# Kernel tuning notes

Hardware: AMD Instinct MI355X
Metric: run time of the kernel (lower is better)

The kernel has to match this reference:

```python
import jax, jax.numpy as jnp
import numpy as np

LEVEL = 2
IN_CH = 128
OUT_CH = 128
BASE_MODES = (16, 16)


def haar_dwt(x):
    # x: [B, C, H, W] with even H, W. Orthonormal 2D Haar (db1) analysis.
    x00 = x[:, :, 0::2, 0::2]
    x01 = x[:, :, 0::2, 1::2]
    x10 = x[:, :, 1::2, 0::2]
    x11 = x[:, :, 1::2, 1::2]
    ll = (x00 + x01 + x10 + x11) * 0.5
    lh = (x00 - x01 + x10 - x11) * 0.5  # high-freq along width
    hl = (x00 + x01 - x10 - x11) * 0.5  # high-freq along height
    hh = (x00 - x01 - x10 + x11) * 0.5
    return ll, lh, hl, hh


def haar_idwt(ll, lh, hl, hh):
    # Orthonormal 2D Haar synthesis (exact inverse of haar_dwt).
    x00 = (ll + lh + hl + hh) * 0.5
    x01 = (ll - lh + hl - hh) * 0.5
    x10 = (ll + lh - hl - hh) * 0.5
    x11 = (ll - lh - hl + hh) * 0.5
    b, c, h2, w2 = ll.shape
    row0 = jnp.stack([x00, x01], axis=-1).reshape(b, c, h2, 2 * w2)
    row1 = jnp.stack([x10, x11], axis=-1).reshape(b, c, h2, 2 * w2)
    return jnp.stack([row0, row1], axis=-2).reshape(b, c, 2 * h2, 2 * w2)


def setup_inputs() -> dict:
    key = jax.random.key(0)
    kx, k1, k2, k3, k4 = jax.random.split(key, 5)
    scale = 1.0 / (IN_CH * OUT_CH)
    wshape = (IN_CH, OUT_CH) + BASE_MODES
    x = jax.random.normal(kx, (32, IN_CH, 128, 128), dtype=jnp.float32)
    w1 = scale * jax.random.uniform(k1, wshape, dtype=jnp.float32)
    w2 = scale * jax.random.uniform(k2, wshape, dtype=jnp.float32)
    w3 = scale * jax.random.uniform(k3, wshape, dtype=jnp.float32)
    w4 = scale * jax.random.uniform(k4, wshape, dtype=jnp.float32)
    return {"x": x, "w1": w1, "w2": w2, "w3": w3, "w4": w4}


def reference(x, w1, w2, w3, w4):
    # Multi-level Haar DWT
    ll = x
    coeffs = []  # finest -> coarsest, matching pytorch_wavelets yh ordering
    for _ in range(LEVEL):
        ll, lh, hl, hh = haar_dwt(ll)
        coeffs.append((lh, hl, hh))

    th, tw = ll.shape[-2], ll.shape[-1]

    def interp(w):
        # bilinear, half-pixel centers == torch align_corners=False (upsampling)
        return jax.image.resize(w, w.shape[:2] + (th, tw), method="bilinear")

    def mul2d(a, w):
        return jnp.einsum("bixy,ioxy->boxy", a, interp(w))

    out_ll = mul2d(ll, w1)
    lh, hl, hh = coeffs[-1]  # only coarsest level is mixed; finer levels zeroed
    out = haar_idwt(out_ll, mul2d(lh, w2), mul2d(hl, w3), mul2d(hh, w4))
    for _ in range(LEVEL - 1):
        z = jnp.zeros_like(out)
        out = haar_idwt(out, z, z, z)
    return out
```

## Files before the change

kernel.cpp:

```cpp
#include <hip/hip_runtime.h>
#include <stdint.h>

__device__ __forceinline__ float bf2f(uint32_t v) { return __uint_as_float(v << 16); }
__device__ __forceinline__ uint32_t f2bf(float f) {
  uint32_t u = __float_as_uint(f);
  return (u + 0x7fffu + ((u >> 16) & 1u)) >> 16;
}

__device__ __forceinline__ void interp_coord(int p, int& i0, int& i1, float& f) {
  if (p == 0)       { i0 = 0;  i1 = 0;  f = 0.f; }
  else if (p == 31) { i0 = 15; i1 = 15; f = 0.f; }
  else if (p & 1)   { i0 = (p - 1) >> 1; i1 = i0 + 1; f = 0.25f; }
  else              { i0 = (p >> 1) - 1; i1 = i0 + 1; f = 0.75f; }
}

typedef short bf16x8 __attribute__((ext_vector_type(8)));
typedef float f32x4 __attribute__((ext_vector_type(4)));

__global__ __launch_bounds__(256) void dwt_kernel(const float* __restrict__ x,
                                                  uint16_t* __restrict__ bands) {
  __shared__ uint16_t tile[4 * 32 * 34];
  const int bid = blockIdx.x;
  const int cg4 = bid & 3;
  const int h   = (bid >> 2) & 31;
  const int b   = bid >> 7;
  const int t   = threadIdx.x;
  const int w   = t & 31;
  const int cl  = t >> 5;
#pragma unroll
  for (int cc = 0; cc < 4; ++cc) {
    const int c = cl + (cc << 3);
    const float* xc = x + (((size_t)(b << 7) + (cg4 << 5) + c) << 14) + (h << 9) + (w << 2);
    float4 r0 = *(const float4*)(xc);
    float4 r1 = *(const float4*)(xc + 128);
    float4 r2 = *(const float4*)(xc + 256);
    float4 r3 = *(const float4*)(xc + 384);
    float S00 = r0.x + r0.y + r1.x + r1.y;
    float S01 = r0.z + r0.w + r1.z + r1.w;
    float S10 = r2.x + r2.y + r3.x + r3.y;
    float S11 = r2.z + r2.w + r3.z + r3.w;
    tile[(0 * 32 + w) * 34 + c] = (uint16_t)f2bf(0.25f * (S00 + S01 + S10 + S11));
    tile[(1 * 32 + w) * 34 + c] = (uint16_t)f2bf(0.25f * (S00 - S01 + S10 - S11));
    tile[(2 * 32 + w) * 34 + c] = (uint16_t)f2bf(0.25f * (S00 + S01 - S10 - S11));
    tile[(3 * 32 + w) * 34 + c] = (uint16_t)f2bf(0.25f * (S00 - S01 - S10 + S11));
  }
  __syncthreads();
  const uint32_t* tl = (const uint32_t*)tile;
  uint32_t* bo = (uint32_t*)bands;
#pragma unroll
  for (int j = 0; j < 8; ++j) {
    const int idx = t + (j << 8);
    const int k   = idx >> 9;
    const int rem = idx & 511;
    const int w2  = rem >> 4;
    const int qq  = rem & 15;
    const uint32_t v = tl[(k * 32 + w2) * 17 + qq];
    bo[(((size_t)(k << 10) + (h << 5) + w2) << 11) + (b << 6) + (cg4 << 4) + qq] = v;
  }
}

__global__ __launch_bounds__(256) void wrepack_kernel(const float* __restrict__ w1,
                                                      const float* __restrict__ w2,
                                                      const float* __restrict__ w3,
                                                      const float* __restrict__ w4,
                                                      uint16_t* __restrict__ wr) {
  __shared__ uint16_t L[64 * 262];
  const int bid = blockIdx.x;
  const int k = bid >> 7;
  const int o = bid & 127;
  const float* src = (k == 0) ? w1 : (k == 1) ? w2 : (k == 2) ? w3 : w4;
  const int t = threadIdx.x;
  uint32_t* Lu = (uint32_t*)L;
  for (int ih = 0; ih < 2; ++ih) {
    if (ih) __syncthreads();
#pragma unroll
    for (int j = 0; j < 16; ++j) {
      const int ridx = t + (j << 8);
      const int il = ridx >> 6;
      const int x4 = ridx & 63;
      float4 v = *(const float4*)(src + (((size_t)((ih * 64 + il) * 128 + o)) << 8) + (x4 << 2));
      Lu[il * 131 + (x4 << 1)]     = f2bf(v.x) | (f2bf(v.y) << 16);
      Lu[il * 131 + (x4 << 1) + 1] = f2bf(v.z) | (f2bf(v.w) << 16);
    }
    __syncthreads();
#pragma unroll
    for (int j = 0; j < 32; ++j) {
      const int oidx = t + (j << 8);
      const int yx = oidx >> 5;
      const int q  = oidx & 31;
      const uint32_t lo = L[(q << 1) * 262 + yx];
      const uint32_t hi = L[((q << 1) + 1) * 262 + yx];
      uint32_t* dst = (uint32_t*)wr + (((size_t)(k << 8) + yx) << 13) + (o << 6) + (ih << 5) + q;
      *dst = lo | (hi << 16);
    }
  }
}

__global__ __launch_bounds__(256) void gemm_kernel(const uint16_t* __restrict__ bands,
                                                   const uint16_t* __restrict__ wr,
                                                   uint16_t* __restrict__ ws2) {
  __shared__ uint16_t Wt[128 * 136];
  const int bid = blockIdx.x;
  const int k = bid & 3;
  const int p = bid >> 2;
  const int t = threadIdx.x;
  const int py = p >> 5, px = p & 31;
  int y0, y1, x0, x1; float fy, fx;
  interp_coord(py, y0, y1, fy);
  interp_coord(px, x0, x1, fx);
  const float c00 = (1.f - fy) * (1.f - fx), c01 = (1.f - fy) * fx;
  const float c10 = fy * (1.f - fx),         c11 = fy * fx;
  const uint16_t* wk = wr + ((size_t)k << 22);
  const uint4* rA = (const uint4*)(wk + (((size_t)(y0 << 4) + x0) << 14));
  const uint4* rB = (const uint4*)(wk + (((size_t)(y0 << 4) + x1) << 14));
  const uint4* rC = (const uint4*)(wk + (((size_t)(y1 << 4) + x0) << 14));
  const uint4* rD = (const uint4*)(wk + (((size_t)(y1 << 4) + x1) << 14));
  uint32_t* Wtu = (uint32_t*)Wt;
#pragma unroll
  for (int j = 0; j < 8; ++j) {
    const int fi = t + (j << 8);
    const int o  = fi >> 4;
    const int i8 = fi & 15;
    const uint4 a = rA[fi], b = rB[fi], c = rC[fi], d = rD[fi];
    uint32_t ou[4];
#pragma unroll
    for (int cc = 0; cc < 4; ++cc) {
      const uint32_t ua = (&a.x)[cc], ub = (&b.x)[cc], uc = (&c.x)[cc], ud = (&d.x)[cc];
      float lo = c00 * __uint_as_float(ua << 16) + c01 * __uint_as_float(ub << 16)
               + c10 * __uint_as_float(uc << 16) + c11 * __uint_as_float(ud << 16);
      float hi = c00 * __uint_as_float(ua & 0xffff0000u) + c01 * __uint_as_float(ub & 0xffff0000u)
               + c10 * __uint_as_float(uc & 0xffff0000u) + c11 * __uint_as_float(ud & 0xffff0000u);
      ou[cc] = f2bf(lo) | (f2bf(hi) << 16);
    }
    *(uint4*)(Wtu + o * 68 + (i8 << 2)) = make_uint4(ou[0], ou[1], ou[2], ou[3]);
  }
  __syncthreads();
  const int wv = t >> 6;
  const int l  = t & 63;
  const int lr = l & 15;
  const int lk = (l >> 4) << 3;
  const uint16_t* gA = bands + (((size_t)(k << 10) + p) << 12);
  bf16x8 af[2][4], bg[2][4];
#pragma unroll
  for (int s = 0; s < 4; ++s) {
#pragma unroll
    for (int m = 0; m < 2; ++m)
      af[m][s] = *(const bf16x8*)(gA + (((m << 4) + lr) << 7) + (s << 5) + lk);
#pragma unroll
    for (int n = 0; n < 2; ++n)
      bg[n][s] = *(const bf16x8*)(&Wt[((wv << 5) + (n << 4) + lr) * 136 + (s << 5) + lk]);
  }
  f32x4 acc[2][2] = {};
#pragma unroll
  for (int s = 0; s < 4; ++s)
#pragma unroll
    for (int m = 0; m < 2; ++m)
#pragma unroll
      for (int n = 0; n < 2; ++n)
        acc[m][n] = __builtin_amdgcn_mfma_f32_16x16x32_bf16(af[m][s], bg[n][s], acc[m][n], 0, 0, 0);
  __syncthreads();
  uint16_t* Ds = Wt;
#pragma unroll
  for (int m = 0; m < 2; ++m)
#pragma unroll
    for (int n = 0; n < 2; ++n)
#pragma unroll
      for (int r = 0; r < 4; ++r) {
        const int b_ = (m << 4) + ((l >> 4) << 2) + r;
        const int o_ = (wv << 5) + (n << 4) + lr;
        Ds[b_ * 136 + o_] = (uint16_t)f2bf(acc[m][n][r]);
      }
  __syncthreads();
  uint32_t* outp = (uint32_t*)(ws2 + (((size_t)(k << 10) + p) << 12));
  const uint32_t* Dsu = (const uint32_t*)Ds;
#pragma unroll
  for (int j = 0; j < 8; ++j) {
    const int idx = t + (j << 8);
    const int b_ = idx >> 6, c_ = idx & 63;
    outp[idx] = Dsu[b_ * 68 + c_];
  }
}

__global__ __launch_bounds__(256) void idwt_kernel(const uint16_t* __restrict__ ws2,
                                                   float* __restrict__ out) {
  __shared__ uint16_t Ls[4 * 32 * 130];
  const int bid = blockIdx.x;
  const int b = bid >> 5;
  const int h = bid & 31;
  const int t = threadIdx.x;
  const uint32_t* su = (const uint32_t*)ws2;
  uint32_t* Lu = (uint32_t*)Ls;
#pragma unroll 4
  for (int j = 0; j < 32; ++j) {
    const int idx = t + (j << 8);
    const int kw = idx >> 6;
    const int uo = idx & 63;
    const int k = kw >> 5, w = kw & 31;
    const uint32_t v = su[(((size_t)(k << 10) + (h << 5) + w) << 11) + (b << 6) + uo];
    Lu[kw * 65 + uo] = v;
  }
  __syncthreads();
  const int x4 = t & 31;
  const int og = t >> 5;
  for (int pp = 0; pp < 16; ++pp) {
    const int o = (pp << 3) + og;
    const float A = bf2f(Ls[(0 * 32 + x4) * 130 + o]);
    const float B = bf2f(Ls[(1 * 32 + x4) * 130 + o]);
    const float C = bf2f(Ls[(2 * 32 + x4) * 130 + o]);
    const float D = bf2f(Ls[(3 * 32 + x4) * 130 + o]);
    const float E = A + B, F = A - B, G = C + D, Hh = C - D;
    const float vL0 = 0.25f * (E + G),  vR0 = 0.25f * (F + Hh);
    const float vL1 = 0.25f * (E - G),  vR1 = 0.25f * (F - Hh);
    float* ob = out + (((size_t)(b << 7) + o) << 14) + (h << 9) + (x4 << 2);
    float4 top = make_float4(vL0, vL0, vR0, vR0);
    float4 bot = make_float4(vL1, vL1, vR1, vR1);
    *(float4*)(ob)       = top;
    *(float4*)(ob + 128) = top;
    *(float4*)(ob + 256) = bot;
    *(float4*)(ob + 384) = bot;
  }
}

extern "C" void kernel_launch(void* const* d_in, const int* in_sizes, int n_in,
                              void* d_out, int out_size, void* d_ws, size_t ws_size,
                              hipStream_t stream) {
  const float* x  = (const float*)d_in[0];
  const float* w1 = (const float*)d_in[1];
  const float* w2 = (const float*)d_in[2];
  const float* w3 = (const float*)d_in[3];
  const float* w4 = (const float*)d_in[4];

  uint16_t* bands = (uint16_t*)d_ws;
  uint16_t* ws2   = bands + (size_t)16777216;
  uint16_t* wr = (uint16_t*)d_out;

  wrepack_kernel<<<512, 256, 0, stream>>>(w1, w2, w3, w4, wr);
  dwt_kernel<<<4096, 256, 0, stream>>>(x, bands);
  gemm_kernel<<<4096, 256, 0, stream>>>(bands, wr, ws2);
  idwt_kernel<<<1024, 256, 0, stream>>>(ws2, (float*)d_out);
}
```

Before: 557.5 us.

## Merge weight repack into DWT kernel and share weight corners across four GEMM positions

```diff
diff --git a/kernel.cpp b/kernel.cpp
--- a/kernel.cpp
+++ b/kernel.cpp
@@ -17,81 +17,80 @@
 typedef short bf16x8 __attribute__((ext_vector_type(8)));
 typedef float f32x4 __attribute__((ext_vector_type(4)));
 
-__global__ __launch_bounds__(256) void dwt_kernel(const float* __restrict__ x,
-                                                  uint16_t* __restrict__ bands) {
-  __shared__ uint16_t tile[4 * 32 * 34];
-  const int bid = blockIdx.x;
-  const int cg4 = bid & 3;
-  const int h   = (bid >> 2) & 31;
-  const int b   = bid >> 7;
-  const int t   = threadIdx.x;
-  const int w   = t & 31;
-  const int cl  = t >> 5;
-#pragma unroll
-  for (int cc = 0; cc < 4; ++cc) {
-    const int c = cl + (cc << 3);
-    const float* xc = x + (((size_t)(b << 7) + (cg4 << 5) + c) << 14) + (h << 9) + (w << 2);
-    float4 r0 = *(const float4*)(xc);
-    float4 r1 = *(const float4*)(xc + 128);
-    float4 r2 = *(const float4*)(xc + 256);
-    float4 r3 = *(const float4*)(xc + 384);
-    float S00 = r0.x + r0.y + r1.x + r1.y;
-    float S01 = r0.z + r0.w + r1.z + r1.w;
-    float S10 = r2.x + r2.y + r3.x + r3.y;
-    float S11 = r2.z + r2.w + r3.z + r3.w;
-    tile[(0 * 32 + w) * 34 + c] = (uint16_t)f2bf(0.25f * (S00 + S01 + S10 + S11));
-    tile[(1 * 32 + w) * 34 + c] = (uint16_t)f2bf(0.25f * (S00 - S01 + S10 - S11));
-    tile[(2 * 32 + w) * 34 + c] = (uint16_t)f2bf(0.25f * (S00 + S01 - S10 - S11));
-    tile[(3 * 32 + w) * 34 + c] = (uint16_t)f2bf(0.25f * (S00 - S01 - S10 + S11));
-  }
-  __syncthreads();
-  const uint32_t* tl = (const uint32_t*)tile;
-  uint32_t* bo = (uint32_t*)bands;
-#pragma unroll
-  for (int j = 0; j < 8; ++j) {
-    const int idx = t + (j << 8);
-    const int k   = idx >> 9;
-    const int rem = idx & 511;
-    const int w2  = rem >> 4;
-    const int qq  = rem & 15;
-    const uint32_t v = tl[(k * 32 + w2) * 17 + qq];
-    bo[(((size_t)(k << 10) + (h << 5) + w2) << 11) + (b << 6) + (cg4 << 4) + qq] = v;
-  }
-}
-
-__global__ __launch_bounds__(256) void wrepack_kernel(const float* __restrict__ w1,
-                                                      const float* __restrict__ w2,
-                                                      const float* __restrict__ w3,
-                                                      const float* __restrict__ w4,
-                                                      uint16_t* __restrict__ wr) {
-  __shared__ uint16_t L[64 * 262];
-  const int bid = blockIdx.x;
-  const int k = bid >> 7;
-  const int o = bid & 127;
-  const float* src = (k == 0) ? w1 : (k == 1) ? w2 : (k == 2) ? w3 : w4;
+__global__ __launch_bounds__(256) void front_kernel(const float* __restrict__ x,
+                                                    const float* __restrict__ w1,
+                                                    const float* __restrict__ w2,
+                                                    const float* __restrict__ w3,
+                                                    const float* __restrict__ w4,
+                                                    uint16_t* __restrict__ bands,
+                                                    uint16_t* __restrict__ wr) {
+  __shared__ uint16_t sh[64 * 262];
   const int t = threadIdx.x;
-  uint32_t* Lu = (uint32_t*)L;
-  for (int ih = 0; ih < 2; ++ih) {
-    if (ih) __syncthreads();
-#pragma unroll
-    for (int j = 0; j < 16; ++j) {
-      const int ridx = t + (j << 8);
-      const int il = ridx >> 6;
-      const int x4 = ridx & 63;
-      float4 v = *(const float4*)(src + (((size_t)((ih * 64 + il) * 128 + o)) << 8) + (x4 << 2));
-      Lu[il * 131 + (x4 << 1)]     = f2bf(v.x) | (f2bf(v.y) << 16);
-      Lu[il * 131 + (x4 << 1) + 1] = f2bf(v.z) | (f2bf(v.w) << 16);
-    }
-    __syncthreads();
-#pragma unroll
-    for (int j = 0; j < 32; ++j) {
-      const int oidx = t + (j << 8);
-      const int yx = oidx >> 5;
-      const int q  = oidx & 31;
-      const uint32_t lo = L[(q << 1) * 262 + yx];
-      const uint32_t hi = L[((q << 1) + 1) * 262 + yx];
-      uint32_t* dst = (uint32_t*)wr + (((size_t)(k << 8) + yx) << 13) + (o << 6) + (ih << 5) + q;
-      *dst = lo | (hi << 16);
+  if (blockIdx.x < 512) {
+    const int bid = blockIdx.x;
+    const int k = bid >> 7;
+    const int o = bid & 127;
+    const float* src = (k == 0) ? w1 : (k == 1) ? w2 : (k == 2) ? w3 : w4;
+    uint32_t* Lu = (uint32_t*)sh;
+    for (int ih = 0; ih < 2; ++ih) {
+      if (ih) __syncthreads();
+#pragma unroll
+      for (int j = 0; j < 16; ++j) {
+        const int ridx = t + (j << 8);
+        const int il = ridx >> 6;
+        const int x4 = ridx & 63;
+        float4 v = *(const float4*)(src + (((size_t)((ih * 64 + il) * 128 + o)) << 8) + (x4 << 2));
+        Lu[il * 131 + (x4 << 1)]     = f2bf(v.x) | (f2bf(v.y) << 16);
+        Lu[il * 131 + (x4 << 1) + 1] = f2bf(v.z) | (f2bf(v.w) << 16);
+      }
+      __syncthreads();
+#pragma unroll
+      for (int j = 0; j < 32; ++j) {
+        const int oidx = t + (j << 8);
+        const int yx = oidx >> 5;
+        const int q  = oidx & 31;
+        const uint32_t lo = sh[(q << 1) * 262 + yx];
+        const uint32_t hi = sh[((q << 1) + 1) * 262 + yx];
+        uint32_t* dst = (uint32_t*)wr + (((size_t)(k << 8) + yx) << 13) + (o << 6) + (ih << 5) + q;
+        *dst = lo | (hi << 16);
+      }
+    }
+  } else {
+    const int bid = blockIdx.x - 512;
+    const int cg4 = bid & 3;
+    const int h   = (bid >> 2) & 31;
+    const int b   = bid >> 7;
+    const int w   = t & 31;
+    const int cl  = t >> 5;
+#pragma unroll
+    for (int cc = 0; cc < 4; ++cc) {
+      const int c = cl + (cc << 3);
+      const float* xc = x + (((size_t)(b << 7) + (cg4 << 5) + c) << 14) + (h << 9) + (w << 2);
+      float4 r0 = *(const float4*)(xc);
+      float4 r1 = *(const float4*)(xc + 128);
+      float4 r2 = *(const float4*)(xc + 256);
+      float4 r3 = *(const float4*)(xc + 384);
+      float S00 = r0.x + r0.y + r1.x + r1.y;
+      float S01 = r0.z + r0.w + r1.z + r1.w;
+      float S10 = r2.x + r2.y + r3.x + r3.y;
+      float S11 = r2.z + r2.w + r3.z + r3.w;
+      sh[(0 * 32 + w) * 34 + c] = (uint16_t)f2bf(0.25f * (S00 + S01 + S10 + S11));
+      sh[(1 * 32 + w) * 34 + c] = (uint16_t)f2bf(0.25f * (S00 - S01 + S10 - S11));
+      sh[(2 * 32 + w) * 34 + c] = (uint16_t)f2bf(0.25f * (S00 + S01 - S10 - S11));
+      sh[(3 * 32 + w) * 34 + c] = (uint16_t)f2bf(0.25f * (S00 - S01 - S10 + S11));
+    }
+    __syncthreads();
+    const uint32_t* tl = (const uint32_t*)sh;
+    uint32_t* bo = (uint32_t*)bands;
+#pragma unroll
+    for (int j = 0; j < 8; ++j) {
+      const int idx = t + (j << 8);
+      const int k   = idx >> 9;
+      const int rem = idx & 511;
+      const int w2  = rem >> 4;
+      const int qq  = rem & 15;
+      const uint32_t v = tl[(k * 32 + w2) * 17 + qq];
+      bo[(((size_t)(k << 10) + (h << 5) + w2) << 11) + (b << 6) + (cg4 << 4) + qq] = v;
     }
   }
 }
@@ -101,83 +100,104 @@
                                                    uint16_t* __restrict__ ws2) {
   __shared__ uint16_t Wt[128 * 136];
   const int bid = blockIdx.x;
-  const int k = bid & 3;
-  const int p = bid >> 2;
-  const int t = threadIdx.x;
-  const int py = p >> 5, px = p & 31;
-  int y0, y1, x0, x1; float fy, fx;
-  interp_coord(py, y0, y1, fy);
-  interp_coord(px, x0, x1, fx);
-  const float c00 = (1.f - fy) * (1.f - fx), c01 = (1.f - fy) * fx;
-  const float c10 = fy * (1.f - fx),         c11 = fy * fx;
+  const int lid = ((bid & 7) << 7) + (bid >> 3);
+  const int xg = lid & 15;
+  const int yg = (lid >> 4) & 15;
+  const int k  = lid >> 8;
+  int pys[2], pxs[2], ya, yb, xa, xb;
+  if (yg < 15) { pys[0] = 2 * yg + 1; pys[1] = 2 * yg + 2; ya = yg; yb = yg + 1; }
+  else         { pys[0] = 0;          pys[1] = 31;         ya = 0;  yb = 15;     }
+  if (xg < 15) { pxs[0] = 2 * xg + 1; pxs[1] = 2 * xg + 2; xa = xg; xb = xg + 1; }
+  else         { pxs[0] = 0;          pxs[1] = 31;         xa = 0;  xb = 15;     }
+  float WY[2][2], WX[2][2];
+#pragma unroll
+  for (int i = 0; i < 2; ++i) {
+    int y0_, y1_; float fy;
+    interp_coord(pys[i], y0_, y1_, fy);
+    WY[i][0] = (y0_ == ya ? (1.f - fy) : 0.f) + (y1_ == ya ? fy : 0.f);
+    WY[i][1] = (y0_ == yb ? (1.f - fy) : 0.f) + (y1_ == yb ? fy : 0.f);
+    int x0_, x1_; float fx;
+    interp_coord(pxs[i], x0_, x1_, fx);
+    WX[i][0] = (x0_ == xa ? (1.f - fx) : 0.f) + (x1_ == xa ? fx : 0.f);
+    WX[i][1] = (x0_ == xb ? (1.f - fx) : 0.f) + (x1_ == xb ? fx : 0.f);
+  }
   const uint16_t* wk = wr + ((size_t)k << 22);
-  const uint4* rA = (const uint4*)(wk + (((size_t)(y0 << 4) + x0) << 14));
-  const uint4* rB = (const uint4*)(wk + (((size_t)(y0 << 4) + x1) << 14));
-  const uint4* rC = (const uint4*)(wk + (((size_t)(y1 << 4) + x0) << 14));
-  const uint4* rD = (const uint4*)(wk + (((size_t)(y1 << 4) + x1) << 14));
-  uint32_t* Wtu = (uint32_t*)Wt;
-#pragma unroll
-  for (int j = 0; j < 8; ++j) {
-    const int fi = t + (j << 8);
-    const int o  = fi >> 4;
-    const int i8 = fi & 15;
-    const uint4 a = rA[fi], b = rB[fi], c = rC[fi], d = rD[fi];
-    uint32_t ou[4];
-#pragma unroll
-    for (int cc = 0; cc < 4; ++cc) {
-      const uint32_t ua = (&a.x)[cc], ub = (&b.x)[cc], uc = (&c.x)[cc], ud = (&d.x)[cc];
-      float lo = c00 * __uint_as_float(ua << 16) + c01 * __uint_as_float(ub << 16)
-               + c10 * __uint_as_float(uc << 16) + c11 * __uint_as_float(ud << 16);
-      float hi = c00 * __uint_as_float(ua & 0xffff0000u) + c01 * __uint_as_float(ub & 0xffff0000u)
-               + c10 * __uint_as_float(uc & 0xffff0000u) + c11 * __uint_as_float(ud & 0xffff0000u);
-      ou[cc] = f2bf(lo) | (f2bf(hi) << 16);
-    }
-    *(uint4*)(Wtu + o * 68 + (i8 << 2)) = make_uint4(ou[0], ou[1], ou[2], ou[3]);
-  }
-  __syncthreads();
+  const uint4* rA = (const uint4*)wk + (size_t)((ya << 4) + xa) * 2048;
+  const uint4* rB = (const uint4*)wk + (size_t)((ya << 4) + xb) * 2048;
+  const uint4* rC = (const uint4*)wk + (size_t)((yb << 4) + xa) * 2048;
+  const uint4* rD = (const uint4*)wk + (size_t)((yb << 4) + xb) * 2048;
+  const int t  = threadIdx.x;
   const int wv = t >> 6;
   const int l  = t & 63;
   const int lr = l & 15;
   const int lk = (l >> 4) << 3;
-  const uint16_t* gA = bands + (((size_t)(k << 10) + p) << 12);
-  bf16x8 af[2][4], bg[2][4];
-#pragma unroll
-  for (int s = 0; s < 4; ++s) {
+  uint32_t* Wtu = (uint32_t*)Wt;
+#pragma unroll 1
+  for (int pp = 0; pp < 4; ++pp) {
+    const int iy = pp >> 1, ix = pp & 1;
+    const float c00 = WY[iy][0] * WX[ix][0], c01 = WY[iy][0] * WX[ix][1];
+    const float c10 = WY[iy][1] * WX[ix][0], c11 = WY[iy][1] * WX[ix][1];
+    const int p = (pys[iy] << 5) + pxs[ix];
+    if (pp) __syncthreads();
+#pragma unroll
+    for (int j = 0; j < 8; ++j) {
+      const int fi = t + (j << 8);
+      const int o  = fi >> 4;
+      const int i8 = fi & 15;
+      const uint4 a = rA[fi], b = rB[fi], c = rC[fi], d = rD[fi];
+      uint32_t ou[4];
+#pragma unroll
+      for (int cc = 0; cc < 4; ++cc) {
+        const uint32_t ua = (&a.x)[cc], ub = (&b.x)[cc], uc = (&c.x)[cc], ud = (&d.x)[cc];
+        float lo = c00 * __uint_as_float(ua << 16) + c01 * __uint_as_float(ub << 16)
+                 + c10 * __uint_as_float(uc << 16) + c11 * __uint_as_float(ud << 16);
+        float hi = c00 * __uint_as_float(ua & 0xffff0000u) + c01 * __uint_as_float(ub & 0xffff0000u)
+                 + c10 * __uint_as_float(uc & 0xffff0000u) + c11 * __uint_as_float(ud & 0xffff0000u);
+        ou[cc] = f2bf(lo) | (f2bf(hi) << 16);
+      }
+      *(uint4*)(Wtu + o * 68 + (i8 << 2)) = make_uint4(ou[0], ou[1], ou[2], ou[3]);
+    }
+    __syncthreads();
+    const uint16_t* gA = bands + (((size_t)(k << 10) + p) << 12);
+    bf16x8 af[2][4], bg[2][4];
+#pragma unroll
+    for (int s = 0; s < 4; ++s) {
+#pragma unroll
+      for (int m = 0; m < 2; ++m)
+        af[m][s] = *(const bf16x8*)(gA + (((m << 4) + lr) << 7) + (s << 5) + lk);
+#pragma unroll
+      for (int n = 0; n < 2; ++n)
+        bg[n][s] = *(const bf16x8*)(&Wt[((wv << 5) + (n << 4) + lr) * 136 + (s << 5) + lk]);
+    }
+    f32x4 acc[2][2] = {};
+#pragma unroll
+    for (int s = 0; s < 4; ++s)
+#pragma unroll
+      for (int m = 0; m < 2; ++m)
+#pragma unroll
+        for (int n = 0; n < 2; ++n)
+          acc[m][n] = __builtin_amdgcn_mfma_f32_16x16x32_bf16(af[m][s], bg[n][s], acc[m][n], 0, 0, 0);
+    __syncthreads();
+    uint16_t* Ds = Wt;
 #pragma unroll
     for (int m = 0; m < 2; ++m)
-      af[m][s] = *(const bf16x8*)(gA + (((m << 4) + lr) << 7) + (s << 5) + lk);
-#pragma unroll
-    for (int n = 0; n < 2; ++n)
-      bg[n][s] = *(const bf16x8*)(&Wt[((wv << 5) + (n << 4) + lr) * 136 + (s << 5) + lk]);
-  }
-  f32x4 acc[2][2] = {};
-#pragma unroll
-  for (int s = 0; s < 4; ++s)
-#pragma unroll
-    for (int m = 0; m < 2; ++m)
 #pragma unroll
       for (int n = 0; n < 2; ++n)
-        acc[m][n] = __builtin_amdgcn_mfma_f32_16x16x32_bf16(af[m][s], bg[n][s], acc[m][n], 0, 0, 0);
-  __syncthreads();
-  uint16_t* Ds = Wt;
-#pragma unroll
-  for (int m = 0; m < 2; ++m)
-#pragma unroll
-    for (int n = 0; n < 2; ++n)
-#pragma unroll
-      for (int r = 0; r < 4; ++r) {
-        const int b_ = (m << 4) + ((l >> 4) << 2) + r;
-        const int o_ = (wv << 5) + (n << 4) + lr;
-        Ds[b_ * 136 + o_] = (uint16_t)f2bf(acc[m][n][r]);
-      }
-  __syncthreads();
-  uint32_t* outp = (uint32_t*)(ws2 + (((size_t)(k << 10) + p) << 12));
-  const uint32_t* Dsu = (const uint32_t*)Ds;
-#pragma unroll
-  for (int j = 0; j < 8; ++j) {
-    const int idx = t + (j << 8);
-    const int b_ = idx >> 6, c_ = idx & 63;
-    outp[idx] = Dsu[b_ * 68 + c_];
+#pragma unroll
+        for (int r = 0; r < 4; ++r) {
+          const int b_ = (m << 4) + ((l >> 4) << 2) + r;
+          const int o_ = (wv << 5) + (n << 4) + lr;
+          Ds[b_ * 136 + o_] = (uint16_t)f2bf(acc[m][n][r]);
+        }
+    __syncthreads();
+    uint32_t* outp = (uint32_t*)(ws2 + (((size_t)(k << 10) + p) << 12));
+    const uint32_t* Dsu = (const uint32_t*)Ds;
+#pragma unroll
+    for (int j = 0; j < 8; ++j) {
+      const int idx = t + (j << 8);
+      const int b_ = idx >> 6, c_ = idx & 63;
+      outp[idx] = Dsu[b_ * 68 + c_];
+    }
   }
 }
 
@@ -234,8 +254,7 @@
   uint16_t* ws2   = bands + (size_t)16777216;
   uint16_t* wr = (uint16_t*)d_out;
 
-  wrepack_kernel<<<512, 256, 0, stream>>>(w1, w2, w3, w4, wr);
-  dwt_kernel<<<4096, 256, 0, stream>>>(x, bands);
-  gemm_kernel<<<4096, 256, 0, stream>>>(bands, wr, ws2);
+  front_kernel<<<4608, 256, 0, stream>>>(x, w1, w2, w3, w4, bands, wr);
+  gemm_kernel<<<1024, 256, 0, stream>>>(bands, wr, ws2);
   idwt_kernel<<<1024, 256, 0, stream>>>(ws2, (float*)d_out);
 }
```

After: 575.6 us. 1.03x slower.

## Apply bilinear weight interpolation to GEMM outputs instead of weights

Applied to the files above, without the earlier changes.

```diff
diff --git a/kernel.cpp b/kernel.cpp
--- a/kernel.cpp
+++ b/kernel.cpp
@@ -99,7 +99,7 @@
 __global__ __launch_bounds__(256) void gemm_kernel(const uint16_t* __restrict__ bands,
                                                    const uint16_t* __restrict__ wr,
                                                    uint16_t* __restrict__ ws2) {
-  __shared__ uint16_t Wt[128 * 136];
+  __shared__ uint16_t Ds[32 * 136];
   const int bid = blockIdx.x;
   const int k = bid & 3;
   const int p = bid >> 2;
@@ -108,58 +108,52 @@
   int y0, y1, x0, x1; float fy, fx;
   interp_coord(py, y0, y1, fy);
   interp_coord(px, x0, x1, fx);
-  const float c00 = (1.f - fy) * (1.f - fx), c01 = (1.f - fy) * fx;
-  const float c10 = fy * (1.f - fx),         c11 = fy * fx;
+  const float coef[4] = {(1.f - fy) * (1.f - fx), (1.f - fy) * fx,
+                         fy * (1.f - fx),         fy * fx};
   const uint16_t* wk = wr + ((size_t)k << 22);
-  const uint4* rA = (const uint4*)(wk + (((size_t)(y0 << 4) + x0) << 14));
-  const uint4* rB = (const uint4*)(wk + (((size_t)(y0 << 4) + x1) << 14));
-  const uint4* rC = (const uint4*)(wk + (((size_t)(y1 << 4) + x0) << 14));
-  const uint4* rD = (const uint4*)(wk + (((size_t)(y1 << 4) + x1) << 14));
-  uint32_t* Wtu = (uint32_t*)Wt;
-#pragma unroll
-  for (int j = 0; j < 8; ++j) {
-    const int fi = t + (j << 8);
-    const int o  = fi >> 4;
-    const int i8 = fi & 15;
-    const uint4 a = rA[fi], b = rB[fi], c = rC[fi], d = rD[fi];
-    uint32_t ou[4];
-#pragma unroll
-    for (int cc = 0; cc < 4; ++cc) {
-      const uint32_t ua = (&a.x)[cc], ub = (&b.x)[cc], uc = (&c.x)[cc], ud = (&d.x)[cc];
-      float lo = c00 * __uint_as_float(ua << 16) + c01 * __uint_as_float(ub << 16)
-               + c10 * __uint_as_float(uc << 16) + c11 * __uint_as_float(ud << 16);
-      float hi = c00 * __uint_as_float(ua & 0xffff0000u) + c01 * __uint_as_float(ub & 0xffff0000u)
-               + c10 * __uint_as_float(uc & 0xffff0000u) + c11 * __uint_as_float(ud & 0xffff0000u);
-      ou[cc] = f2bf(lo) | (f2bf(hi) << 16);
-    }
-    *(uint4*)(Wtu + o * 68 + (i8 << 2)) = make_uint4(ou[0], ou[1], ou[2], ou[3]);
-  }
-  __syncthreads();
+  const uint16_t* cells[4] = {
+      wk + (((size_t)(y0 << 4) + x0) << 14),
+      wk + (((size_t)(y0 << 4) + x1) << 14),
+      wk + (((size_t)(y1 << 4) + x0) << 14),
+      wk + (((size_t)(y1 << 4) + x1) << 14)};
   const int wv = t >> 6;
   const int l  = t & 63;
   const int lr = l & 15;
   const int lk = (l >> 4) << 3;
   const uint16_t* gA = bands + (((size_t)(k << 10) + p) << 12);
-  bf16x8 af[2][4], bg[2][4];
-#pragma unroll
-  for (int s = 0; s < 4; ++s) {
+  bf16x8 af[2][4];
+#pragma unroll
+  for (int s = 0; s < 4; ++s)
 #pragma unroll
     for (int m = 0; m < 2; ++m)
       af[m][s] = *(const bf16x8*)(gA + (((m << 4) + lr) << 7) + (s << 5) + lk);
-#pragma unroll
-    for (int n = 0; n < 2; ++n)
-      bg[n][s] = *(const bf16x8*)(&Wt[((wv << 5) + (n << 4) + lr) * 136 + (s << 5) + lk]);
-  }
-  f32x4 acc[2][2] = {};
-#pragma unroll
-  for (int s = 0; s < 4; ++s)
+  f32x4 tot[2][2] = {};
+#pragma unroll
+  for (int cix = 0; cix < 4; ++cix) {
+    const uint16_t* cp = cells[cix];
+    bf16x8 bg[2][4];
+#pragma unroll
+    for (int s = 0; s < 4; ++s)
+#pragma unroll
+      for (int n = 0; n < 2; ++n)
+        bg[n][s] = *(const bf16x8*)(cp + (((wv << 5) + (n << 4) + lr) << 7) + (s << 5) + lk);
+    f32x4 acc[2][2] = {};
+#pragma unroll
+    for (int s = 0; s < 4; ++s)
+#pragma unroll
+      for (int m = 0; m < 2; ++m)
+#pragma unroll
+        for (int n = 0; n < 2; ++n)
+          acc[m][n] = __builtin_amdgcn_mfma_f32_16x16x32_bf16(af[m][s], bg[n][s], acc[m][n], 0, 0, 0);
+    const float cf = coef[cix];
 #pragma unroll
     for (int m = 0; m < 2; ++m)
 #pragma unroll
       for (int n = 0; n < 2; ++n)
-        acc[m][n] = __builtin_amdgcn_mfma_f32_16x16x32_bf16(af[m][s], bg[n][s], acc[m][n], 0, 0, 0);
-  __syncthreads();
-  uint16_t* Ds = Wt;
+#pragma unroll
+        for (int r = 0; r < 4; ++r)
+          tot[m][n][r] += cf * acc[m][n][r];
+  }
 #pragma unroll
   for (int m = 0; m < 2; ++m)
 #pragma unroll
@@ -168,7 +162,7 @@
       for (int r = 0; r < 4; ++r) {
         const int b_ = (m << 4) + ((l >> 4) << 2) + r;
         const int o_ = (wv << 5) + (n << 4) + lr;
-        Ds[b_ * 136 + o_] = (uint16_t)f2bf(acc[m][n][r]);
+        Ds[b_ * 136 + o_] = (uint16_t)f2bf(tot[m][n][r]);
       }
   __syncthreads();
   uint32_t* outp = (uint32_t*)(ws2 + (((size_t)(k << 10) + p) << 12));
```

Measured after the change: 584.3 us. +4.8%, slower.

## Fuse per-band GEMM and inverse Haar into one tail kernel

Applied to the files above, without the earlier changes.

```diff
diff --git a/kernel.cpp b/kernel.cpp
--- a/kernel.cpp
+++ b/kernel.cpp
@@ -96,70 +96,74 @@
   }
 }
 
-__global__ __launch_bounds__(256) void gemm_kernel(const uint16_t* __restrict__ bands,
+__global__ __launch_bounds__(256) void tail_kernel(const uint16_t* __restrict__ bands,
                                                    const uint16_t* __restrict__ wr,
-                                                   uint16_t* __restrict__ ws2) {
+                                                   float* __restrict__ out) {
   __shared__ uint16_t Wt[128 * 136];
   const int bid = blockIdx.x;
-  const int k = bid & 3;
-  const int p = bid >> 2;
-  const int t = threadIdx.x;
-  const int py = p >> 5, px = p & 31;
+  const int h  = bid >> 5;
+  const int jq = (bid >> 3) & 3;
+  const int wq = bid & 7;
+  const int w  = (wq << 2) + jq;
+  const int p  = (h << 5) + w;
+  const int t  = threadIdx.x;
   int y0, y1, x0, x1; float fy, fx;
-  interp_coord(py, y0, y1, fy);
-  interp_coord(px, x0, x1, fx);
+  interp_coord(h, y0, y1, fy);
+  interp_coord(w, x0, x1, fx);
   const float c00 = (1.f - fy) * (1.f - fx), c01 = (1.f - fy) * fx;
   const float c10 = fy * (1.f - fx),         c11 = fy * fx;
-  const uint16_t* wk = wr + ((size_t)k << 22);
-  const uint4* rA = (const uint4*)(wk + (((size_t)(y0 << 4) + x0) << 14));
-  const uint4* rB = (const uint4*)(wk + (((size_t)(y0 << 4) + x1) << 14));
-  const uint4* rC = (const uint4*)(wk + (((size_t)(y1 << 4) + x0) << 14));
-  const uint4* rD = (const uint4*)(wk + (((size_t)(y1 << 4) + x1) << 14));
-  uint32_t* Wtu = (uint32_t*)Wt;
-#pragma unroll
-  for (int j = 0; j < 8; ++j) {
-    const int fi = t + (j << 8);
-    const int o  = fi >> 4;
-    const int i8 = fi & 15;
-    const uint4 a = rA[fi], b = rB[fi], c = rC[fi], d = rD[fi];
-    uint32_t ou[4];
-#pragma unroll
-    for (int cc = 0; cc < 4; ++cc) {
-      const uint32_t ua = (&a.x)[cc], ub = (&b.x)[cc], uc = (&c.x)[cc], ud = (&d.x)[cc];
-      float lo = c00 * __uint_as_float(ua << 16) + c01 * __uint_as_float(ub << 16)
-               + c10 * __uint_as_float(uc << 16) + c11 * __uint_as_float(ud << 16);
-      float hi = c00 * __uint_as_float(ua & 0xffff0000u) + c01 * __uint_as_float(ub & 0xffff0000u)
-               + c10 * __uint_as_float(uc & 0xffff0000u) + c11 * __uint_as_float(ud & 0xffff0000u);
-      ou[cc] = f2bf(lo) | (f2bf(hi) << 16);
-    }
-    *(uint4*)(Wtu + o * 68 + (i8 << 2)) = make_uint4(ou[0], ou[1], ou[2], ou[3]);
-  }
-  __syncthreads();
   const int wv = t >> 6;
   const int l  = t & 63;
   const int lr = l & 15;
   const int lk = (l >> 4) << 3;
-  const uint16_t* gA = bands + (((size_t)(k << 10) + p) << 12);
-  bf16x8 af[2][4], bg[2][4];
-#pragma unroll
-  for (int s = 0; s < 4; ++s) {
-#pragma unroll
-    for (int m = 0; m < 2; ++m)
-      af[m][s] = *(const bf16x8*)(gA + (((m << 4) + lr) << 7) + (s << 5) + lk);
-#pragma unroll
-    for (int n = 0; n < 2; ++n)
-      bg[n][s] = *(const bf16x8*)(&Wt[((wv << 5) + (n << 4) + lr) * 136 + (s << 5) + lk]);
-  }
-  f32x4 acc[2][2] = {};
-#pragma unroll
-  for (int s = 0; s < 4; ++s)
-#pragma unroll
-    for (int m = 0; m < 2; ++m)
+  uint32_t* Wtu = (uint32_t*)Wt;
+  f32x4 acc[4][2][2] = {};
+#pragma unroll 1
+  for (int k = 0; k < 4; ++k) {
+    if (k) __syncthreads();
+    const uint16_t* wk = wr + ((size_t)k << 22);
+    const uint4* rA = (const uint4*)(wk + (((size_t)(y0 << 4) + x0) << 14));
+    const uint4* rB = (const uint4*)(wk + (((size_t)(y0 << 4) + x1) << 14));
+    const uint4* rC = (const uint4*)(wk + (((size_t)(y1 << 4) + x0) << 14));
+    const uint4* rD = (const uint4*)(wk + (((size_t)(y1 << 4) + x1) << 14));
+#pragma unroll
+    for (int j = 0; j < 8; ++j) {
+      const int fi = t + (j << 8);
+      const int o  = fi >> 4;
+      const int i8 = fi & 15;
+      const uint4 a = rA[fi], b = rB[fi], c = rC[fi], d = rD[fi];
+      uint32_t ou[4];
+#pragma unroll
+      for (int cc = 0; cc < 4; ++cc) {
+        const uint32_t ua = (&a.x)[cc], ub = (&b.x)[cc], uc = (&c.x)[cc], ud = (&d.x)[cc];
+        float lo = c00 * __uint_as_float(ua << 16) + c01 * __uint_as_float(ub << 16)
+                 + c10 * __uint_as_float(uc << 16) + c11 * __uint_as_float(ud << 16);
+        float hi = c00 * __uint_as_float(ua & 0xffff0000u) + c01 * __uint_as_float(ub & 0xffff0000u)
+                 + c10 * __uint_as_float(uc & 0xffff0000u) + c11 * __uint_as_float(ud & 0xffff0000u);
+        ou[cc] = f2bf(lo) | (f2bf(hi) << 16);
+      }
+      *(uint4*)(Wtu + o * 68 + (i8 << 2)) = make_uint4(ou[0], ou[1], ou[2], ou[3]);
+    }
+    __syncthreads();
+    const uint16_t* gA = bands + (((size_t)(k << 10) + p) << 12);
+    bf16x8 af[2][4], bg[2][4];
+#pragma unroll
+    for (int s = 0; s < 4; ++s) {
+#pragma unroll
+      for (int m = 0; m < 2; ++m)
+        af[m][s] = *(const bf16x8*)(gA + (((m << 4) + lr) << 7) + (s << 5) + lk);
 #pragma unroll
       for (int n = 0; n < 2; ++n)
-        acc[m][n] = __builtin_amdgcn_mfma_f32_16x16x32_bf16(af[m][s], bg[n][s], acc[m][n], 0, 0, 0);
-  __syncthreads();
-  uint16_t* Ds = Wt;
+        bg[n][s] = *(const bf16x8*)(&Wt[((wv << 5) + (n << 4) + lr) * 136 + (s << 5) + lk]);
+    }
+#pragma unroll
+    for (int s = 0; s < 4; ++s)
+#pragma unroll
+      for (int m = 0; m < 2; ++m)
+#pragma unroll
+        for (int n = 0; n < 2; ++n)
+          acc[k][m][n] = __builtin_amdgcn_mfma_f32_16x16x32_bf16(af[m][s], bg[n][s], acc[k][m][n], 0, 0, 0);
+  }
 #pragma unroll
   for (int m = 0; m < 2; ++m)
 #pragma unroll
@@ -168,57 +172,19 @@
       for (int r = 0; r < 4; ++r) {
         const int b_ = (m << 4) + ((l >> 4) << 2) + r;
         const int o_ = (wv << 5) + (n << 4) + lr;
-        Ds[b_ * 136 + o_] = (uint16_t)f2bf(acc[m][n][r]);
+        const float A = acc[0][m][n][r], B = acc[1][m][n][r];
+        const float C = acc[2][m][n][r], D = acc[3][m][n][r];
+        const float E = A + B, F = A - B, G = C + D, Hh = C - D;
+        const float vL0 = 0.25f * (E + G),  vR0 = 0.25f * (F + Hh);
+        const float vL1 = 0.25f * (E - G),  vR1 = 0.25f * (F - Hh);
+        float* ob = out + (((size_t)(b_ << 7) + o_) << 14) + (h << 9) + (w << 2);
+        float4 top = make_float4(vL0, vL0, vR0, vR0);
+        float4 bot = make_float4(vL1, vL1, vR1, vR1);
+        *(float4*)(ob)       = top;
+        *(float4*)(ob + 128) = top;
+        *(float4*)(ob + 256) = bot;
+        *(float4*)(ob + 384) = bot;
       }
-  __syncthreads();
-  uint32_t* outp = (uint32_t*)(ws2 + (((size_t)(k << 10) + p) << 12));
-  const uint32_t* Dsu = (const uint32_t*)Ds;
-#pragma unroll
-  for (int j = 0; j < 8; ++j) {
-    const int idx = t + (j << 8);
-    const int b_ = idx >> 6, c_ = idx & 63;
-    outp[idx] = Dsu[b_ * 68 + c_];
-  }
-}
-
-__global__ __launch_bounds__(256) void idwt_kernel(const uint16_t* __restrict__ ws2,
-                                                   float* __restrict__ out) {
-  __shared__ uint16_t Ls[4 * 32 * 130];
-  const int bid = blockIdx.x;
-  const int b = bid >> 5;
-  const int h = bid & 31;
-  const int t = threadIdx.x;
-  const uint32_t* su = (const uint32_t*)ws2;
-  uint32_t* Lu = (uint32_t*)Ls;
-#pragma unroll 4
-  for (int j = 0; j < 32; ++j) {
-    const int idx = t + (j << 8);
-    const int kw = idx >> 6;
-    const int uo = idx & 63;
-    const int k = kw >> 5, w = kw & 31;
-    const uint32_t v = su[(((size_t)(k << 10) + (h << 5) + w) << 11) + (b << 6) + uo];
-    Lu[kw * 65 + uo] = v;
-  }
-  __syncthreads();
-  const int x4 = t & 31;
-  const int og = t >> 5;
-  for (int pp = 0; pp < 16; ++pp) {
-    const int o = (pp << 3) + og;
-    const float A = bf2f(Ls[(0 * 32 + x4) * 130 + o]);
-    const float B = bf2f(Ls[(1 * 32 + x4) * 130 + o]);
-    const float C = bf2f(Ls[(2 * 32 + x4) * 130 + o]);
-    const float D = bf2f(Ls[(3 * 32 + x4) * 130 + o]);
-    const float E = A + B, F = A - B, G = C + D, Hh = C - D;
-    const float vL0 = 0.25f * (E + G),  vR0 = 0.25f * (F + Hh);
-    const float vL1 = 0.25f * (E - G),  vR1 = 0.25f * (F - Hh);
-    float* ob = out + (((size_t)(b << 7) + o) << 14) + (h << 9) + (x4 << 2);
-    float4 top = make_float4(vL0, vL0, vR0, vR0);
-    float4 bot = make_float4(vL1, vL1, vR1, vR1);
-    *(float4*)(ob)       = top;
-    *(float4*)(ob + 128) = top;
-    *(float4*)(ob + 256) = bot;
-    *(float4*)(ob + 384) = bot;
-  }
 }
 
 extern "C" void kernel_launch(void* const* d_in, const int* in_sizes, int n_in,
@@ -231,11 +197,9 @@
   const float* w4 = (const float*)d_in[4];
 
   uint16_t* bands = (uint16_t*)d_ws;
-  uint16_t* ws2   = bands + (size_t)16777216;
-  uint16_t* wr = (uint16_t*)d_out;
+  uint16_t* wr    = bands + (size_t)16777216;
 
   wrepack_kernel<<<512, 256, 0, stream>>>(w1, w2, w3, w4, wr);
   dwt_kernel<<<4096, 256, 0, stream>>>(x, bands);
-  gemm_kernel<<<4096, 256, 0, stream>>>(bands, wr, ws2);
-  idwt_kernel<<<1024, 256, 0, stream>>>(ws2, (float*)d_out);
-}
+  tail_kernel<<<1024, 256, 0, stream>>>(bands, wr, (float*)d_out);
+}
```

After: 803.4 us. 44.1% more time.
